# Kernel optimization log

Hardware: AMD Instinct MI355X
Metric: run time of the kernel (lower is better)

The kernel has to match this reference:

```python
import jax, jax.numpy as jnp
import numpy as np

B, S, D, E, K, DFF = 4, 2048, 1024, 8, 2, 2048  # d_ffn = 4*D//K rounded to block_size=128 -> 2048


def setup_inputs() -> dict:
    key = jax.random.key(0)
    k1, k2, k3, k4 = jax.random.split(key, 4)
    x = jax.random.normal(k1, (B, S, D), dtype=jnp.float32)
    # router: nn.Linear(D, E, bias=False) -> weight applied as x @ W^T; store as [D, E]
    router_w = jax.random.normal(k2, (D, E), dtype=jnp.float32) * 0.02
    # trunc_normal(std=0.02, a=-0.06, b=0.06) ~ clipped normal
    w1 = jnp.clip(jax.random.normal(k3, (D, DFF * E), dtype=jnp.float32) * 0.02, -0.06, 0.06)
    w2 = jnp.clip(jax.random.normal(k4, (DFF * E, D), dtype=jnp.float32) * 0.02, -0.06, 0.06)
    return {"x": x, "router_w": router_w, "w1": w1, "w2": w2}


def reference(x, router_w, w1, w2):
    b, s, d = x.shape
    x_flat = x.reshape(-1, d)                      # [T, D]
    T = x_flat.shape[0]

    # --- routing (softmax in fp32, top-k, renormalize) ---
    router_logits = x_flat @ router_w              # [T, E]
    probs = jax.nn.softmax(router_logits.astype(jnp.float32), axis=-1)
    rw, sel = jax.lax.top_k(probs, K)              # [T, K]
    rw = rw / jnp.sum(rw, axis=-1, keepdims=True)  # norm_topk_prob=True
    rw = rw.astype(x.dtype)

    # dense gate matrix [T, E]: top-k weight where selected, else 0
    gates = jnp.zeros((T, E), dtype=x.dtype).at[jnp.arange(T)[:, None], sel].add(rw)

    # --- grouped expert FFN (equivalent to sort/pad + block-sparse SDD/GELU/DSD) ---
    # w1[:, e*DFF:(e+1)*DFF] and w2[e*DFF:(e+1)*DFF, :] are expert e's weights.
    out = jnp.zeros((T, d), dtype=x.dtype)
    for e in range(E):                             # small fixed loop over experts
        h = jax.nn.gelu(x_flat @ w1[:, e * DFF:(e + 1) * DFF], approximate=False)
        out = out + gates[:, e:e + 1] * (h @ w2[e * DFF:(e + 1) * DFF, :])

    return out.reshape(b, s, d)
```

## Files before the change

### kernel.cpp

```cpp
#include <hip/hip_runtime.h>
#include <hip/hip_bf16.h>

#define T_TOK 8192
#define D_DIM 1024
#define E_NUM 8
#define TOPK 2
#define DFF_DIM 2048
#define BM 128
#define BK 64
#define MAX_TILES 136
#define MAX_PAIRS_PAD (MAX_TILES*BM)

typedef __attribute__((ext_vector_type(8))) short short8_t;
typedef __attribute__((ext_vector_type(4))) float f32x4;

__device__ __forceinline__ unsigned short f2b(float f) {
  union { float f; unsigned u; } v; v.f = f;
  unsigned u = v.u;
  return (unsigned short)((u + 0x7fffu + ((u >> 16) & 1u)) >> 16);
}

__device__ __forceinline__ void gload_lds16(const void* g, void* l) {
  __builtin_amdgcn_global_load_lds(
      (const __attribute__((address_space(1))) unsigned int*)g,
      (__attribute__((address_space(3))) unsigned int*)l, 16, 0, 0);
}

__global__ void tcvt_kernel(const float* __restrict__ src, unsigned short* __restrict__ dst,
                            int R, int C) {
  __shared__ float tile[32][33];
  int c0 = blockIdx.x * 32, r0 = blockIdx.y * 32;
  int tx = threadIdx.x, ty = threadIdx.y;
  #pragma unroll
  for (int i = 0; i < 32; i += 8)
    tile[ty + i][tx] = src[(size_t)(r0 + ty + i) * C + c0 + tx];
  __syncthreads();
  #pragma unroll
  for (int i = 0; i < 32; i += 8)
    dst[(size_t)(c0 + ty + i) * R + r0 + tx] = f2b(tile[tx][ty + i]);
}

__global__ void router_kernel(const float* __restrict__ x, const float* __restrict__ rw,
                              int* __restrict__ sel, float* __restrict__ selw,
                              unsigned short* __restrict__ xb) {
  int tok = (blockIdx.x * blockDim.x + threadIdx.x) >> 6;
  int lane = threadIdx.x & 63;
  if (tok >= T_TOK) return;
  const float4* xr = (const float4*)(x + (size_t)tok * D_DIM);
  ushort4* xbr = (ushort4*)(xb + (size_t)tok * D_DIM);
  float acc[E_NUM];
  #pragma unroll
  for (int e = 0; e < E_NUM; ++e) acc[e] = 0.f;
  #pragma unroll
  for (int it = 0; it < 4; ++it) {
    int i = it * 64 + lane;
    float4 v = xr[i];
    ushort4 o;
    o.x = f2b(v.x); o.y = f2b(v.y); o.z = f2b(v.z); o.w = f2b(v.w);
    xbr[i] = o;
    const float* w = rw + (size_t)i * 4 * E_NUM;
    #pragma unroll
    for (int e = 0; e < E_NUM; ++e) acc[e] += v.x * w[e];
    #pragma unroll
    for (int e = 0; e < E_NUM; ++e) acc[e] += v.y * w[E_NUM + e];
    #pragma unroll
    for (int e = 0; e < E_NUM; ++e) acc[e] += v.z * w[2 * E_NUM + e];
    #pragma unroll
    for (int e = 0; e < E_NUM; ++e) acc[e] += v.w * w[3 * E_NUM + e];
  }
  #pragma unroll
  for (int e = 0; e < E_NUM; ++e) {
    float v = acc[e];
    #pragma unroll
    for (int off = 32; off > 0; off >>= 1) v += __shfl_xor(v, off, 64);
    acc[e] = v;
  }
  if (lane == 0) {
    float mx = acc[0];
    #pragma unroll
    for (int e = 1; e < E_NUM; ++e) mx = fmaxf(mx, acc[e]);
    float p[E_NUM];
    #pragma unroll
    for (int e = 0; e < E_NUM; ++e) p[e] = __expf(acc[e] - mx);
    int i0 = 0;
    #pragma unroll
    for (int e = 1; e < E_NUM; ++e) if (p[e] > p[i0]) i0 = e;
    int i1 = (i0 == 0) ? 1 : 0;
    #pragma unroll
    for (int e = 0; e < E_NUM; ++e) if (e != i0 && p[e] > p[i1]) i1 = e;
    float w0 = p[i0], w1 = p[i1];
    float inv = 1.f / (w0 + w1);
    sel[tok * 2] = i0; selw[tok * 2] = w0 * inv;
    sel[tok * 2 + 1] = i1; selw[tok * 2 + 1] = w1 * inv;
  }
}

__global__ void count_kernel(const int* __restrict__ sel, int* __restrict__ counts) {
  __shared__ int lc[E_NUM];
  if (threadIdx.x < E_NUM) lc[threadIdx.x] = 0;
  __syncthreads();
  int t = blockIdx.x * blockDim.x + threadIdx.x;
  if (t < 2 * T_TOK) atomicAdd(&lc[sel[t]], 1);
  __syncthreads();
  if (threadIdx.x < E_NUM) atomicAdd(&counts[threadIdx.x], lc[threadIdx.x]);
}

__global__ void plan_kernel(const int* __restrict__ counts, int* __restrict__ tiles_e,
                            int* __restrict__ tiles_b, int* __restrict__ pad_off,
                            int* __restrict__ cursor, int* __restrict__ ptok,
                            float* __restrict__ pgate, unsigned short* __restrict__ zpad) {
  if (threadIdx.x == 0) {
    int b = 0, t = 0;
    for (int e = 0; e < E_NUM; ++e) {
      pad_off[e] = b;
      int nt = (counts[e] + BM - 1) >> 7;
      for (int i = 0; i < nt; ++i) { tiles_e[t] = e; tiles_b[t] = b + i * BM; ++t; }
      b += nt * BM;
    }
    for (; t < MAX_TILES; ++t) { tiles_e[t] = -1; tiles_b[t] = 0; }
  }
  for (int i = threadIdx.x; i < MAX_PAIRS_PAD; i += blockDim.x) { ptok[i] = -1; pgate[i] = 0.f; }
  for (int i = threadIdx.x; i < 64; i += blockDim.x) zpad[i] = 0;
  if (threadIdx.x < E_NUM) cursor[threadIdx.x] = 0;
}

__global__ void scatter_kernel(const int* __restrict__ sel, const float* __restrict__ selw,
                               const int* __restrict__ pad_off, int* __restrict__ cursor,
                               int* __restrict__ ptok, float* __restrict__ pgate) {
  __shared__ int lc[E_NUM];
  __shared__ int lbase[E_NUM];
  if (threadIdx.x < E_NUM) lc[threadIdx.x] = 0;
  __syncthreads();
  int t = blockIdx.x * blockDim.x + threadIdx.x;
  int e0 = sel[t * 2], e1 = sel[t * 2 + 1];
  int o0 = atomicAdd(&lc[e0], 1);
  int o1 = atomicAdd(&lc[e1], 1);
  __syncthreads();
  if (threadIdx.x < E_NUM) lbase[threadIdx.x] = atomicAdd(&cursor[threadIdx.x], lc[threadIdx.x]);
  __syncthreads();
  int s0 = pad_off[e0] + lbase[e0] + o0;
  ptok[s0] = t; pgate[s0] = selw[t * 2];
  int s1 = pad_off[e1] + lbase[e1] + o1;
  ptok[s1] = t; pgate[s1] = selw[t * 2 + 1];
}

__global__ __launch_bounds__(256, 2) void gemm1_kernel(
    const unsigned short* __restrict__ xb, const unsigned short* __restrict__ w1t,
    const int* __restrict__ ptok, const int* __restrict__ tiles_e,
    const int* __restrict__ tiles_b, const unsigned short* __restrict__ zpad,
    unsigned short* __restrict__ h) {
  const int e = tiles_e[blockIdx.y];
  if (e < 0) return;
  const int base = tiles_b[blockIdx.y];
  const int n0 = blockIdx.x * 128;

  __shared__ unsigned short As[BM * BK];
  __shared__ unsigned short Bs[BM * BK];

  const int tid = threadIdx.x;
  const int lane = tid & 63;
  const int wv = tid >> 6;
  const int wr = wv >> 1, wc = wv & 1;

  int atok[4], aoff[4];
  const unsigned short* bptr[4];
  #pragma unroll
  for (int i = 0; i < 4; ++i) {
    int c = i * 256 + tid;
    int row = c >> 3, kc = c & 7;
    atok[i] = ptok[base + row];
    aoff[i] = kc * 8;
    bptr[i] = w1t + (size_t)(e * DFF_DIM + n0 + row) * D_DIM + kc * 8;
  }

  f32x4 acc[4][4];
  #pragma unroll
  for (int m = 0; m < 4; ++m)
    #pragma unroll
    for (int n = 0; n < 4; ++n) acc[m][n] = (f32x4){0.f, 0.f, 0.f, 0.f};

  for (int k0 = 0; k0 < D_DIM; k0 += BK) {
    #pragma unroll
    for (int i = 0; i < 4; ++i) {
      const unsigned short* ga =
          (atok[i] >= 0) ? (xb + (size_t)atok[i] * D_DIM + k0 + aoff[i]) : zpad;
      gload_lds16(ga, &As[(i * 256 + tid) * 8]);
      gload_lds16(bptr[i] + k0, &Bs[(i * 256 + tid) * 8]);
    }
    __syncthreads();
    const int lr = lane & 15;
    const int lk = (lane >> 4) * 8;
    #pragma unroll
    for (int kk = 0; kk < BK; kk += 32) {
      short8_t aF[4], bF[4];
      #pragma unroll
      for (int m = 0; m < 4; ++m)
        aF[m] = *(const short8_t*)&As[(wr * 64 + m * 16 + lr) * BK + kk + lk];
      #pragma unroll
      for (int n = 0; n < 4; ++n)
        bF[n] = *(const short8_t*)&Bs[(wc * 64 + n * 16 + lr) * BK + kk + lk];
      #pragma unroll
      for (int m = 0; m < 4; ++m)
        #pragma unroll
        for (int n = 0; n < 4; ++n)
          acc[m][n] = __builtin_amdgcn_mfma_f32_16x16x32_bf16(aF[m], bF[n], acc[m][n], 0, 0, 0);
    }
    __syncthreads();
  }

  const int lr = lane & 15, lq = lane >> 4;
  #pragma unroll
  for (int m = 0; m < 4; ++m) {
    #pragma unroll
    for (int n = 0; n < 4; ++n) {
      const int col = n0 + wc * 64 + n * 16 + lr;
      #pragma unroll
      for (int j = 0; j < 4; ++j) {
        const int row = base + wr * 64 + m * 16 + lq * 4 + j;
        float v = acc[m][n][j];
        float gl = 0.5f * v * (1.f + erff(v * 0.70710678118654752f));
        h[(size_t)row * DFF_DIM + col] = f2b(gl);
      }
    }
  }
}

__global__ __launch_bounds__(256, 2) void gemm2_kernel(
    const unsigned short* __restrict__ h, const unsigned short* __restrict__ w2t,
    const int* __restrict__ ptok, const float* __restrict__ pgate,
    const int* __restrict__ tiles_e, const int* __restrict__ tiles_b,
    float* __restrict__ out) {
  const int e = tiles_e[blockIdx.y];
  if (e < 0) return;
  const int base = tiles_b[blockIdx.y];
  const int n0 = blockIdx.x * 128;

  __shared__ unsigned short As[BM * BK];
  __shared__ unsigned short Bs[BM * BK];

  const int tid = threadIdx.x;
  const int lane = tid & 63;
  const int wv = tid >> 6;
  const int wr = wv >> 1, wc = wv & 1;

  const unsigned short* aptr[4];
  const unsigned short* bptr[4];
  #pragma unroll
  for (int i = 0; i < 4; ++i) {
    int c = i * 256 + tid;
    int row = c >> 3, kc = c & 7;
    aptr[i] = h + (size_t)(base + row) * DFF_DIM + kc * 8;
    bptr[i] = w2t + (size_t)(n0 + row) * (E_NUM * DFF_DIM) + e * DFF_DIM + kc * 8;
  }

  f32x4 acc[4][4];
  #pragma unroll
  for (int m = 0; m < 4; ++m)
    #pragma unroll
    for (int n = 0; n < 4; ++n) acc[m][n] = (f32x4){0.f, 0.f, 0.f, 0.f};

  for (int k0 = 0; k0 < DFF_DIM; k0 += BK) {
    #pragma unroll
    for (int i = 0; i < 4; ++i) {
      gload_lds16(aptr[i] + k0, &As[(i * 256 + tid) * 8]);
      gload_lds16(bptr[i] + k0, &Bs[(i * 256 + tid) * 8]);
    }
    __syncthreads();
    const int lr = lane & 15;
    const int lk = (lane >> 4) * 8;
    #pragma unroll
    for (int kk = 0; kk < BK; kk += 32) {
      short8_t aF[4], bF[4];
      #pragma unroll
      for (int m = 0; m < 4; ++m)
        aF[m] = *(const short8_t*)&As[(wr * 64 + m * 16 + lr) * BK + kk + lk];
      #pragma unroll
      for (int n = 0; n < 4; ++n)
        bF[n] = *(const short8_t*)&Bs[(wc * 64 + n * 16 + lr) * BK + kk + lk];
      #pragma unroll
      for (int m = 0; m < 4; ++m)
        #pragma unroll
        for (int n = 0; n < 4; ++n)
          acc[m][n] = __builtin_amdgcn_mfma_f32_16x16x32_bf16(aF[m], bF[n], acc[m][n], 0, 0, 0);
    }
    __syncthreads();
  }

  const int lr = lane & 15, lq = lane >> 4;
  #pragma unroll
  for (int m = 0; m < 4; ++m) {
    #pragma unroll
    for (int j = 0; j < 4; ++j) {
      const int p = base + wr * 64 + m * 16 + lq * 4 + j;
      const int tok = ptok[p];
      if (tok < 0) continue;
      const float g = pgate[p];
      #pragma unroll
      for (int n = 0; n < 4; ++n) {
        const int col = n0 + wc * 64 + n * 16 + lr;
        atomicAdd(&out[(size_t)tok * D_DIM + col], g * acc[m][n][j]);
      }
    }
  }
}

extern "C" void kernel_launch(void* const* d_in, const int* in_sizes, int n_in,
                              void* d_out, int out_size, void* d_ws, size_t ws_size,
                              hipStream_t stream) {
  const float* x  = (const float*)d_in[0];
  const float* rw = (const float*)d_in[1];
  const float* w1 = (const float*)d_in[2];
  const float* w2 = (const float*)d_in[3];
  float* out = (float*)d_out;

  char* ws = (char*)d_ws;
  unsigned short* xb   = (unsigned short*)(ws);
  unsigned short* w1t  = (unsigned short*)(ws + 16777216);
  unsigned short* w2t  = (unsigned short*)(ws + 50331648);
  unsigned short* h    = (unsigned short*)(ws + 83886080);
  int*   ptok   = (int*)(ws + 155189248);
  float* pgate  = (float*)(ws + 155258880);
  int*   sel    = (int*)(ws + 155328512);
  float* selw   = (float*)(ws + 155394048);
  int*   counts = (int*)(ws + 155459584);
  int*   cursor = counts + 8;
  int*   padoff = counts + 16;
  int*   tiles_e = counts + 24;
  int*   tiles_b = tiles_e + MAX_TILES;
  unsigned short* zpad = (unsigned short*)(tiles_b + MAX_TILES);
  const size_t WS_NEED = 155459584 + 4096;
  if (ws_size < WS_NEED) return;

  hipMemsetAsync(out, 0, (size_t)T_TOK * D_DIM * sizeof(float), stream);
  hipMemsetAsync(counts, 0, E_NUM * sizeof(int), stream);

  tcvt_kernel<<<dim3(16384 / 32, 1024 / 32), dim3(32, 8), 0, stream>>>(w1, w1t, 1024, 16384);
  tcvt_kernel<<<dim3(1024 / 32, 16384 / 32), dim3(32, 8), 0, stream>>>(w2, w2t, 16384, 1024);
  router_kernel<<<T_TOK / 4, 256, 0, stream>>>(x, rw, sel, selw, xb);
  count_kernel<<<2 * T_TOK / 256, 256, 0, stream>>>(sel, counts);
  plan_kernel<<<1, 256, 0, stream>>>(counts, tiles_e, tiles_b, padoff, cursor, ptok, pgate, zpad);
  scatter_kernel<<<T_TOK / 256, 256, 0, stream>>>(sel, selw, padoff, cursor, ptok, pgate);
  gemm1_kernel<<<dim3(DFF_DIM / 128, MAX_TILES), 256, 0, stream>>>(xb, w1t, ptok, tiles_e,
                                                                   tiles_b, zpad, h);
  gemm2_kernel<<<dim3(D_DIM / 128, MAX_TILES), 256, 0, stream>>>(h, w2t, ptok, pgate, tiles_e,
                                                                 tiles_b, out);
}
```

Before: 357.7 us.

## Use 256-row tiles with double-buffered LDS prefetch in both expert GEMMs

Both grouped GEMMs now use 256-row M tiles with 512 threads (8 waves), and GEMM1 also uses 256-wide N tiles. Each K step's global-to-LDS loads are double-buffered in dynamic shared memory so the next tile loads while the current one is computed. Padding is now per 128 rows, and the new tile limits skip rows past each expert's range; a zero row replaces the small zero pad. The aim is more reuse per LDS load and hidden load latency. The cost is large LDS use (128KB and 96KB), which limits occupancy, plus more waste on the last partial tile of each expert.

```diff
diff --git a/kernel.cpp b/kernel.cpp
--- a/kernel.cpp
+++ b/kernel.cpp
@@ -6,10 +6,8 @@
 #define E_NUM 8
 #define TOPK 2
 #define DFF_DIM 2048
-#define BM 128
-#define BK 64
-#define MAX_TILES 136
-#define MAX_PAIRS_PAD (MAX_TILES*BM)
+#define MAX_PAIRS_PAD 17408
+#define MAX_TILES256 72
 
 typedef __attribute__((ext_vector_type(8))) short short8_t;
 typedef __attribute__((ext_vector_type(4))) float f32x4;
@@ -106,21 +104,25 @@
 }
 
 __global__ void plan_kernel(const int* __restrict__ counts, int* __restrict__ tiles_e,
-                            int* __restrict__ tiles_b, int* __restrict__ pad_off,
-                            int* __restrict__ cursor, int* __restrict__ ptok,
-                            float* __restrict__ pgate, unsigned short* __restrict__ zpad) {
+                            int* __restrict__ tiles_b, int* __restrict__ tiles_l,
+                            int* __restrict__ pad_off, int* __restrict__ cursor,
+                            int* __restrict__ ptok, float* __restrict__ pgate,
+                            unsigned short* __restrict__ zrow) {
   if (threadIdx.x == 0) {
     int b = 0, t = 0;
     for (int e = 0; e < E_NUM; ++e) {
       pad_off[e] = b;
-      int nt = (counts[e] + BM - 1) >> 7;
-      for (int i = 0; i < nt; ++i) { tiles_e[t] = e; tiles_b[t] = b + i * BM; ++t; }
-      b += nt * BM;
-    }
-    for (; t < MAX_TILES; ++t) { tiles_e[t] = -1; tiles_b[t] = 0; }
+      int p128 = ((counts[e] + 127) >> 7) << 7;
+      int nt = (p128 + 255) >> 8;
+      for (int i = 0; i < nt; ++i) {
+        tiles_e[t] = e; tiles_b[t] = b + i * 256; tiles_l[t] = b + p128; ++t;
+      }
+      b += p128;
+    }
+    for (; t < MAX_TILES256; ++t) { tiles_e[t] = -1; tiles_b[t] = 0; tiles_l[t] = 0; }
   }
   for (int i = threadIdx.x; i < MAX_PAIRS_PAD; i += blockDim.x) { ptok[i] = -1; pgate[i] = 0.f; }
-  for (int i = threadIdx.x; i < 64; i += blockDim.x) zpad[i] = 0;
+  for (int i = threadIdx.x; i < 1040; i += blockDim.x) zrow[i] = 0;
   if (threadIdx.x < E_NUM) cursor[threadIdx.x] = 0;
 }
 
@@ -144,33 +146,136 @@
   ptok[s1] = t; pgate[s1] = selw[t * 2 + 1];
 }
 
-__global__ __launch_bounds__(256, 2) void gemm1_kernel(
+__global__ __launch_bounds__(512, 2) void gemm1_kernel(
     const unsigned short* __restrict__ xb, const unsigned short* __restrict__ w1t,
     const int* __restrict__ ptok, const int* __restrict__ tiles_e,
-    const int* __restrict__ tiles_b, const unsigned short* __restrict__ zpad,
-    unsigned short* __restrict__ h) {
+    const int* __restrict__ tiles_b, const int* __restrict__ tiles_l,
+    const unsigned short* __restrict__ zrow, unsigned short* __restrict__ h) {
   const int e = tiles_e[blockIdx.y];
   if (e < 0) return;
-  const int base = tiles_b[blockIdx.y];
+  const int tbase = tiles_b[blockIdx.y];
+  const int tlim = tiles_l[blockIdx.y];
+  const int n0 = blockIdx.x * 256;
+
+  extern __shared__ char smem[];
+
+  const int tid = threadIdx.x;
+  const int lane = tid & 63;
+  const int wv = tid >> 6;
+  const int wr = wv >> 2, wc = wv & 3;
+  const int lr = lane & 15;
+  const int lk8 = (lane >> 4) * 8;
+
+  const unsigned short* asrc[4];
+  const unsigned short* bsrc[4];
+  #pragma unroll
+  for (int i = 0; i < 4; ++i) {
+    int c = i * 512 + tid;
+    int row = c >> 3, c8 = c & 7;
+    int slot = tbase + row; if (slot > MAX_PAIRS_PAD - 1) slot = MAX_PAIRS_PAD - 1;
+    int tok = ptok[slot];
+    asrc[i] = (tok >= 0) ? (xb + (size_t)tok * D_DIM + c8 * 8) : (zrow + c8 * 8);
+    bsrc[i] = w1t + (size_t)(e * DFF_DIM + n0 + row) * D_DIM + c8 * 8;
+  }
+
+  f32x4 acc[8][4];
+  #pragma unroll
+  for (int m = 0; m < 8; ++m)
+    #pragma unroll
+    for (int n = 0; n < 4; ++n) acc[m][n] = (f32x4){0.f, 0.f, 0.f, 0.f};
+
+  #pragma unroll
+  for (int i = 0; i < 4; ++i) {
+    gload_lds16(asrc[i], smem + (i * 512 + tid) * 16);
+    gload_lds16(bsrc[i], smem + 32768 + (i * 512 + tid) * 16);
+  }
+  __syncthreads();
+
+  int cur = 0;
+  const int NT = D_DIM / 64;
+  for (int t = 0; t < NT; ++t) {
+    if (t + 1 < NT) {
+      const int k0n = (t + 1) * 64;
+      char* dst = smem + (cur ^ 1) * 65536;
+      #pragma unroll
+      for (int i = 0; i < 4; ++i) {
+        gload_lds16(asrc[i] + k0n, dst + (i * 512 + tid) * 16);
+        gload_lds16(bsrc[i] + k0n, dst + 32768 + (i * 512 + tid) * 16);
+      }
+    }
+    const unsigned short* Ab = (const unsigned short*)(smem + cur * 65536);
+    const unsigned short* Bb = (const unsigned short*)(smem + cur * 65536 + 32768);
+    #pragma unroll
+    for (int kk = 0; kk < 64; kk += 32) {
+      short8_t aF[8], bF[4];
+      #pragma unroll
+      for (int m = 0; m < 8; ++m)
+        aF[m] = *(const short8_t*)&Ab[(wr * 128 + m * 16 + lr) * 64 + kk + lk8];
+      #pragma unroll
+      for (int n = 0; n < 4; ++n)
+        bF[n] = *(const short8_t*)&Bb[(wc * 64 + n * 16 + lr) * 64 + kk + lk8];
+      #pragma unroll
+      for (int m = 0; m < 8; ++m)
+        #pragma unroll
+        for (int n = 0; n < 4; ++n)
+          acc[m][n] = __builtin_amdgcn_mfma_f32_16x16x32_bf16(aF[m], bF[n], acc[m][n], 0, 0, 0);
+    }
+    __syncthreads();
+    cur ^= 1;
+  }
+
+  const int lq = lane >> 4;
+  #pragma unroll
+  for (int m = 0; m < 8; ++m) {
+    #pragma unroll
+    for (int j = 0; j < 4; ++j) {
+      const int grow = tbase + wr * 128 + m * 16 + lq * 4 + j;
+      if (grow >= tlim) continue;
+      #pragma unroll
+      for (int n = 0; n < 4; ++n) {
+        const int col = n0 + wc * 64 + n * 16 + lr;
+        float v = acc[m][n][j];
+        float gl = 0.5f * v * (1.f + erff(v * 0.70710678118654752f));
+        h[(size_t)grow * DFF_DIM + col] = f2b(gl);
+      }
+    }
+  }
+}
+
+__global__ __launch_bounds__(512, 2) void gemm2_kernel(
+    const unsigned short* __restrict__ h, const unsigned short* __restrict__ w2t,
+    const int* __restrict__ ptok, const float* __restrict__ pgate,
+    const int* __restrict__ tiles_e, const int* __restrict__ tiles_b,
+    const int* __restrict__ tiles_l, float* __restrict__ out) {
+  const int e = tiles_e[blockIdx.y];
+  if (e < 0) return;
+  const int tbase = tiles_b[blockIdx.y];
+  const int tlim = tiles_l[blockIdx.y];
   const int n0 = blockIdx.x * 128;
 
-  __shared__ unsigned short As[BM * BK];
-  __shared__ unsigned short Bs[BM * BK];
+  extern __shared__ char smem[];
 
   const int tid = threadIdx.x;
   const int lane = tid & 63;
   const int wv = tid >> 6;
   const int wr = wv >> 1, wc = wv & 1;
-
-  int atok[4], aoff[4];
-  const unsigned short* bptr[4];
+  const int lr = lane & 15;
+  const int lk8 = (lane >> 4) * 8;
+
+  const unsigned short* asrc[4];
+  const unsigned short* bsrc[2];
   #pragma unroll
   for (int i = 0; i < 4; ++i) {
-    int c = i * 256 + tid;
-    int row = c >> 3, kc = c & 7;
-    atok[i] = ptok[base + row];
-    aoff[i] = kc * 8;
-    bptr[i] = w1t + (size_t)(e * DFF_DIM + n0 + row) * D_DIM + kc * 8;
+    int c = i * 512 + tid;
+    int row = c >> 3, c8 = c & 7;
+    int slot = tbase + row; if (slot > MAX_PAIRS_PAD - 1) slot = MAX_PAIRS_PAD - 1;
+    asrc[i] = h + (size_t)slot * DFF_DIM + c8 * 8;
+  }
+  #pragma unroll
+  for (int j = 0; j < 2; ++j) {
+    int c = j * 512 + tid;
+    int row = c >> 3, c8 = c & 7;
+    bsrc[j] = w2t + (size_t)(n0 + row) * (E_NUM * DFF_DIM) + e * DFF_DIM + c8 * 8;
   }
 
   f32x4 acc[4][4];
@@ -179,26 +284,34 @@
     #pragma unroll
     for (int n = 0; n < 4; ++n) acc[m][n] = (f32x4){0.f, 0.f, 0.f, 0.f};
 
-  for (int k0 = 0; k0 < D_DIM; k0 += BK) {
-    #pragma unroll
-    for (int i = 0; i < 4; ++i) {
-      const unsigned short* ga =
-          (atok[i] >= 0) ? (xb + (size_t)atok[i] * D_DIM + k0 + aoff[i]) : zpad;
-      gload_lds16(ga, &As[(i * 256 + tid) * 8]);
-      gload_lds16(bptr[i] + k0, &Bs[(i * 256 + tid) * 8]);
-    }
-    __syncthreads();
-    const int lr = lane & 15;
-    const int lk = (lane >> 4) * 8;
-    #pragma unroll
-    for (int kk = 0; kk < BK; kk += 32) {
+  #pragma unroll
+  for (int i = 0; i < 4; ++i) gload_lds16(asrc[i], smem + (i * 512 + tid) * 16);
+  #pragma unroll
+  for (int j = 0; j < 2; ++j) gload_lds16(bsrc[j], smem + 32768 + (j * 512 + tid) * 16);
+  __syncthreads();
+
+  int cur = 0;
+  const int NT = DFF_DIM / 64;
+  for (int t = 0; t < NT; ++t) {
+    if (t + 1 < NT) {
+      const int k0n = (t + 1) * 64;
+      char* dst = smem + (cur ^ 1) * 49152;
+      #pragma unroll
+      for (int i = 0; i < 4; ++i) gload_lds16(asrc[i] + k0n, dst + (i * 512 + tid) * 16);
+      #pragma unroll
+      for (int j = 0; j < 2; ++j) gload_lds16(bsrc[j] + k0n, dst + 32768 + (j * 512 + tid) * 16);
+    }
+    const unsigned short* Ab = (const unsigned short*)(smem + cur * 49152);
+    const unsigned short* Bb = (const unsigned short*)(smem + cur * 49152 + 32768);
+    #pragma unroll
+    for (int kk = 0; kk < 64; kk += 32) {
       short8_t aF[4], bF[4];
       #pragma unroll
       for (int m = 0; m < 4; ++m)
-        aF[m] = *(const short8_t*)&As[(wr * 64 + m * 16 + lr) * BK + kk + lk];
+        aF[m] = *(const short8_t*)&Ab[(wr * 64 + m * 16 + lr) * 64 + kk + lk8];
       #pragma unroll
       for (int n = 0; n < 4; ++n)
-        bF[n] = *(const short8_t*)&Bs[(wc * 64 + n * 16 + lr) * BK + kk + lk];
+        bF[n] = *(const short8_t*)&Bb[(wc * 64 + n * 16 + lr) * 64 + kk + lk8];
       #pragma unroll
       for (int m = 0; m < 4; ++m)
         #pragma unroll
@@ -206,92 +319,16 @@
           acc[m][n] = __builtin_amdgcn_mfma_f32_16x16x32_bf16(aF[m], bF[n], acc[m][n], 0, 0, 0);
     }
     __syncthreads();
-  }
-
-  const int lr = lane & 15, lq = lane >> 4;
+    cur ^= 1;
+  }
+
+  const int lq = lane >> 4;
   #pragma unroll
   for (int m = 0; m < 4; ++m) {
     #pragma unroll
-    for (int n = 0; n < 4; ++n) {
-      const int col = n0 + wc * 64 + n * 16 + lr;
-      #pragma unroll
-      for (int j = 0; j < 4; ++j) {
-        const int row = base + wr * 64 + m * 16 + lq * 4 + j;
-        float v = acc[m][n][j];
-        float gl = 0.5f * v * (1.f + erff(v * 0.70710678118654752f));
-        h[(size_t)row * DFF_DIM + col] = f2b(gl);
-      }
-    }
-  }
-}
-
-__global__ __launch_bounds__(256, 2) void gemm2_kernel(
-    const unsigned short* __restrict__ h, const unsigned short* __restrict__ w2t,
-    const int* __restrict__ ptok, const float* __restrict__ pgate,
-    const int* __restrict__ tiles_e, const int* __restrict__ tiles_b,
-    float* __restrict__ out) {
-  const int e = tiles_e[blockIdx.y];
-  if (e < 0) return;
-  const int base = tiles_b[blockIdx.y];
-  const int n0 = blockIdx.x * 128;
-
-  __shared__ unsigned short As[BM * BK];
-  __shared__ unsigned short Bs[BM * BK];
-
-  const int tid = threadIdx.x;
-  const int lane = tid & 63;
-  const int wv = tid >> 6;
-  const int wr = wv >> 1, wc = wv & 1;
-
-  const unsigned short* aptr[4];
-  const unsigned short* bptr[4];
-  #pragma unroll
-  for (int i = 0; i < 4; ++i) {
-    int c = i * 256 + tid;
-    int row = c >> 3, kc = c & 7;
-    aptr[i] = h + (size_t)(base + row) * DFF_DIM + kc * 8;
-    bptr[i] = w2t + (size_t)(n0 + row) * (E_NUM * DFF_DIM) + e * DFF_DIM + kc * 8;
-  }
-
-  f32x4 acc[4][4];
-  #pragma unroll
-  for (int m = 0; m < 4; ++m)
-    #pragma unroll
-    for (int n = 0; n < 4; ++n) acc[m][n] = (f32x4){0.f, 0.f, 0.f, 0.f};
-
-  for (int k0 = 0; k0 < DFF_DIM; k0 += BK) {
-    #pragma unroll
-    for (int i = 0; i < 4; ++i) {
-      gload_lds16(aptr[i] + k0, &As[(i * 256 + tid) * 8]);
-      gload_lds16(bptr[i] + k0, &Bs[(i * 256 + tid) * 8]);
-    }
-    __syncthreads();
-    const int lr = lane & 15;
-    const int lk = (lane >> 4) * 8;
-    #pragma unroll
-    for (int kk = 0; kk < BK; kk += 32) {
-      short8_t aF[4], bF[4];
-      #pragma unroll
-      for (int m = 0; m < 4; ++m)
-        aF[m] = *(const short8_t*)&As[(wr * 64 + m * 16 + lr) * BK + kk + lk];
-      #pragma unroll
-      for (int n = 0; n < 4; ++n)
-        bF[n] = *(const short8_t*)&Bs[(wc * 64 + n * 16 + lr) * BK + kk + lk];
-      #pragma unroll
-      for (int m = 0; m < 4; ++m)
-        #pragma unroll
-        for (int n = 0; n < 4; ++n)
-          acc[m][n] = __builtin_amdgcn_mfma_f32_16x16x32_bf16(aF[m], bF[n], acc[m][n], 0, 0, 0);
-    }
-    __syncthreads();
-  }
-
-  const int lr = lane & 15, lq = lane >> 4;
-  #pragma unroll
-  for (int m = 0; m < 4; ++m) {
-    #pragma unroll
     for (int j = 0; j < 4; ++j) {
-      const int p = base + wr * 64 + m * 16 + lq * 4 + j;
+      const int p = tbase + wr * 64 + m * 16 + lq * 4 + j;
+      if (p >= tlim) continue;
       const int tok = ptok[p];
       if (tok < 0) continue;
       const float g = pgate[p];
@@ -326,10 +363,16 @@
   int*   cursor = counts + 8;
   int*   padoff = counts + 16;
   int*   tiles_e = counts + 24;
-  int*   tiles_b = tiles_e + MAX_TILES;
-  unsigned short* zpad = (unsigned short*)(tiles_b + MAX_TILES);
+  int*   tiles_b = tiles_e + MAX_TILES256;
+  int*   tiles_l = tiles_b + MAX_TILES256;
+  unsigned short* zrow = (unsigned short*)(tiles_l + MAX_TILES256);
   const size_t WS_NEED = 155459584 + 4096;
   if (ws_size < WS_NEED) return;
+
+  hipFuncSetAttribute((const void*)gemm1_kernel,
+                      hipFuncAttributeMaxDynamicSharedMemorySize, 131072);
+  hipFuncSetAttribute((const void*)gemm2_kernel,
+                      hipFuncAttributeMaxDynamicSharedMemorySize, 98304);
 
   hipMemsetAsync(out, 0, (size_t)T_TOK * D_DIM * sizeof(float), stream);
   hipMemsetAsync(counts, 0, E_NUM * sizeof(int), stream);
@@ -338,10 +381,11 @@
   tcvt_kernel<<<dim3(1024 / 32, 16384 / 32), dim3(32, 8), 0, stream>>>(w2, w2t, 16384, 1024);
   router_kernel<<<T_TOK / 4, 256, 0, stream>>>(x, rw, sel, selw, xb);
   count_kernel<<<2 * T_TOK / 256, 256, 0, stream>>>(sel, counts);
-  plan_kernel<<<1, 256, 0, stream>>>(counts, tiles_e, tiles_b, padoff, cursor, ptok, pgate, zpad);
+  plan_kernel<<<1, 256, 0, stream>>>(counts, tiles_e, tiles_b, tiles_l, padoff, cursor,
+                                     ptok, pgate, zrow);
   scatter_kernel<<<T_TOK / 256, 256, 0, stream>>>(sel, selw, padoff, cursor, ptok, pgate);
-  gemm1_kernel<<<dim3(DFF_DIM / 128, MAX_TILES), 256, 0, stream>>>(xb, w1t, ptok, tiles_e,
-                                                                   tiles_b, zpad, h);
-  gemm2_kernel<<<dim3(D_DIM / 128, MAX_TILES), 256, 0, stream>>>(h, w2t, ptok, pgate, tiles_e,
-                                                                 tiles_b, out);
-}
+  gemm1_kernel<<<dim3(DFF_DIM / 256, MAX_TILES256), 512, 131072, stream>>>(
+      xb, w1t, ptok, tiles_e, tiles_b, tiles_l, zrow, h);
+  gemm2_kernel<<<dim3(D_DIM / 128, MAX_TILES256), 512, 98304, stream>>>(
+      h, w2t, ptok, pgate, tiles_e, tiles_b, tiles_l, out);
+}
```

Measured after the change: 424.4 us. +18.6%, slower.
